# Kernel tuning notes

Hardware: AMD Instinct MI355X
Metric: run time of the kernel (lower is better)

Reference implementation:

```python
import jax, jax.numpy as jnp
import numpy as np

B, S, T = 64, 128, 64
HD, VS, VT = 1024, 32000, 32000


def setup_inputs() -> dict:
    key = jax.random.key(0)
    ks = jax.random.split(key, 20)
    p = lambda k, shape: (jax.random.normal(k, shape, jnp.float32) * 0.02)
    return {
        "src_nums": jax.random.randint(ks[0], (B, S), 0, VS, dtype=jnp.int32),
        "tgt_nums": jax.random.randint(ks[1], (B, T), 0, VT, dtype=jnp.int32),
        "src_emb": p(ks[2], (VS, HD)),
        "tgt_emb": p(ks[3], (VT, HD)),
        "enc_Wx1": p(ks[4], (HD, 4 * HD)),
        "enc_Wh1": p(ks[5], (HD, 4 * HD)),
        "enc_b1": jnp.zeros((4 * HD,), jnp.float32),
        "enc_Wx2": p(ks[6], (HD, 4 * HD)),
        "enc_Wh2": p(ks[7], (HD, 4 * HD)),
        "enc_b2": jnp.zeros((4 * HD,), jnp.float32),
        "dec_Wx": p(ks[8], (HD, 4 * HD)),
        "dec_Wh": p(ks[9], (HD, 4 * HD)),
        "dec_b": jnp.zeros((4 * HD,), jnp.float32),
        "dec_h0": p(ks[10], (1, HD)),
        "dec_m0": p(ks[11], (1, HD)),
        "Wt": p(ks[12], (2 * HD, HD)),
        "bt": jnp.zeros((HD,), jnp.float32),
        "Wo": p(ks[13], (HD, VT)),
        "bo": jnp.zeros((VT,), jnp.float32),
    }


def _lstm_cell(x, h, c, Wx, Wh, b):
    g = x @ Wx + h @ Wh + b            # [B, 4H], gate order i,f,g,o
    i, f, gg, o = jnp.split(g, 4, axis=-1)
    c = jax.nn.sigmoid(f) * c + jax.nn.sigmoid(i) * jnp.tanh(gg)
    h = jax.nn.sigmoid(o) * jnp.tanh(c)
    return h, c


def reference(src_nums, tgt_nums, src_emb, tgt_emb,
              enc_Wx1, enc_Wh1, enc_b1, enc_Wx2, enc_Wh2, enc_b2,
              dec_Wx, dec_Wh, dec_b, dec_h0, dec_m0, Wt, bt, Wo, bo):
    Bb, Ss = src_nums.shape
    Hd = src_emb.shape[1]
    # ---- Encoder: 2-layer LSTM over source ----
    embs = src_emb[src_nums]                       # [B,S,H]
    z0 = jnp.zeros((Bb, Hd), embs.dtype)

    def enc_step(carry, x):
        h1, c1, h2, c2 = carry
        h1, c1 = _lstm_cell(x, h1, c1, enc_Wx1, enc_Wh1, enc_b1)
        h2, c2 = _lstm_cell(h1, h2, c2, enc_Wx2, enc_Wh2, enc_b2)
        return (h1, c1, h2, c2), h2

    _, Hseq = jax.lax.scan(enc_step, (z0, z0, z0, z0), jnp.swapaxes(embs, 0, 1))
    Henc = jnp.swapaxes(Hseq, 0, 1)                # [B,S,H]
    mask = src_nums == 0                           # pad mask
    scale = 1.0 / jnp.sqrt(jnp.array(Hd, jnp.float32))

    # ---- Decoder: per-step attention + LSTMCell + tanh proj + log-softmax ----
    h = jnp.tile(dec_h0, (Bb, 1))
    m = jnp.tile(dec_m0, (Bb, 1))

    def dec_step(carry, tgt):
        h, m, loss = carry
        scores = jnp.einsum('bd,bsd->bs', h, Henc) * scale
        scores = jnp.where(mask, -jnp.inf, scores)
        a = jax.nn.softmax(scores, axis=-1)
        ctx = jnp.einsum('bs,bsd->bd', a, Henc)
        z = jnp.tanh(jnp.concatenate([ctx, h], axis=-1) @ Wt + bt)
        logp = jax.nn.log_softmax(z @ Wo + bo, axis=-1)    # [B,V]
        tok_lp = jnp.take_along_axis(logp, tgt[:, None], axis=-1)[:, 0]
        loss = loss - jnp.sum(jnp.where(tgt != 0, tok_lp, 0.0))
        x = tgt_emb[tgt]
        h, m = _lstm_cell(x, h, m, dec_Wx, dec_Wh, dec_b)
        return (h, m, loss), None

    (_, _, loss), _ = jax.lax.scan(
        dec_step, (h, m, jnp.float32(0.0)), jnp.swapaxes(tgt_nums, 0, 1))
    return loss
```

## Files before the change

kernel.cpp:

```cpp
#include <hip/hip_runtime.h>


#define Bv 64
#define Sv 128
#define Tv 64
#define Hv 1024
#define H4v 4096
#define Vv 32000
#define NBLK 256

using bf16x8 = __attribute__((ext_vector_type(8))) short;
using f32x4  = __attribute__((ext_vector_type(4))) float;

typedef __attribute__((address_space(1))) const void gvoid_t;
typedef __attribute__((address_space(3))) void lvoid_t;

__device__ __forceinline__ void gload16(const void* g, void* l) {
  __builtin_amdgcn_global_load_lds((gvoid_t*)g, (lvoid_t*)l, 16, 0, 0);
}

__device__ __forceinline__ float bf2f(unsigned short u) {
  unsigned int v = ((unsigned int)u) << 16;
  return __uint_as_float(v);
}
__device__ __forceinline__ unsigned short f2bf(float f) {
  unsigned int u = __float_as_uint(f);
  return (unsigned short)((u + 0x7FFFu + ((u >> 16) & 1u)) >> 16);
}
__device__ __forceinline__ float sigm(float x) { return 1.f / (1.f + __expf(-x)); }
__device__ __forceinline__ float tanh_f(float x) {
  float ax = fabsf(x);
  float e = __expf(-2.f * ax);
  float t = (1.f - e) / (1.f + e);
  return copysignf(t, x);
}

__device__ __forceinline__ int4 ldx4(const unsigned short* p) {
  int4 r;
  asm volatile("global_load_dwordx4 %0, %1, off" : "=v"(r) : "v"(p));
  return r;
}
__device__ __forceinline__ int2 ldx2(const unsigned short* p) {
  int2 r;
  asm volatile("global_load_dwordx2 %0, %1, off" : "=v"(r) : "v"(p));
  return r;
}
__device__ __forceinline__ void stx2u_wt(unsigned short* p, int2 v) {
  asm volatile("global_store_dwordx2 %0, %1, off sc0 sc1" :: "v"(p), "v"(v) : "memory");
}
__device__ __forceinline__ void vm_wait_c(int n) {
  switch (n) {
    case 32: asm volatile("s_waitcnt vmcnt(32)" ::: "memory"); break;
    case 28: asm volatile("s_waitcnt vmcnt(28)" ::: "memory"); break;
    case 24: asm volatile("s_waitcnt vmcnt(24)" ::: "memory"); break;
    case 20: asm volatile("s_waitcnt vmcnt(20)" ::: "memory"); break;
    case 16: asm volatile("s_waitcnt vmcnt(16)" ::: "memory"); break;
    case 12: asm volatile("s_waitcnt vmcnt(12)" ::: "memory"); break;
    case 8:  asm volatile("s_waitcnt vmcnt(8)"  ::: "memory"); break;
    case 4:  asm volatile("s_waitcnt vmcnt(4)"  ::: "memory"); break;
    default: asm volatile("s_waitcnt vmcnt(0)"  ::: "memory"); break;
  }
}

__device__ __forceinline__ void wait_all64(int* f, int tid) {
  if (tid < 64) {
    int it = 0;
    while (true) {
      int v = __hip_atomic_load(f + tid, __ATOMIC_RELAXED, __HIP_MEMORY_SCOPE_AGENT);
      if (__all(v != 0)) break;
      __builtin_amdgcn_s_sleep(2);
      if (++it > (1 << 17)) break;
    }
  }
  __syncthreads();
}
__device__ __forceinline__ void wait_all128(int* f, int tid) {
  if (tid < 64) {
    int it = 0;
    while (true) {
      int a = __hip_atomic_load(f + tid, __ATOMIC_RELAXED, __HIP_MEMORY_SCOPE_AGENT);
      int b = __hip_atomic_load(f + tid + 64, __ATOMIC_RELAXED, __HIP_MEMORY_SCOPE_AGENT);
      if (__all((a != 0) && (b != 0))) break;
      __builtin_amdgcn_s_sleep(2);
      if (++it > (1 << 17)) break;
    }
  }
  __syncthreads();
}
__device__ __forceinline__ void post_flag(int* f, int tid) {
  __syncthreads();
  if (tid == 0) __hip_atomic_store(f, 1, __ATOMIC_RELAXED, __HIP_MEMORY_SCOPE_AGENT);
}

__global__ __launch_bounds__(256) void transpose_bf16(const float* __restrict__ in,
                                                      unsigned short* __restrict__ out,
                                                      int R, int C, int ostride) {
  __shared__ float tile[32][33];
  int tx = threadIdx.x, ty = threadIdx.y;
  int c0 = blockIdx.x * 32, r0 = blockIdx.y * 32;
#pragma unroll
  for (int i = 0; i < 32; i += 8)
    tile[ty + i][tx] = in[(size_t)(r0 + ty + i) * C + c0 + tx];
  __syncthreads();
#pragma unroll
  for (int i = 0; i < 32; i += 8)
    out[(size_t)(c0 + ty + i) * ostride + r0 + tx] = f2bf(tile[tx][ty + i]);
}

__global__ __launch_bounds__(256) void gather_emb(const int* __restrict__ toks,
                                                  const float* __restrict__ emb,
                                                  unsigned short* __restrict__ dst) {
  int r = blockIdx.x, tid = threadIdx.x;
  int tok = toks[r];
  int j = tid * 4;
  float4 v = *(const float4*)&emb[(size_t)tok * Hv + j];
  ushort4 o;
  o.x = f2bf(v.x); o.y = f2bf(v.y); o.z = f2bf(v.z); o.w = f2bf(v.w);
  *(ushort4*)&dst[(size_t)r * Hv + j] = o;
}

__global__ __launch_bounds__(256) void init_k(unsigned short* __restrict__ zhx,
                                              unsigned short* __restrict__ hdx0,
                                              const float* __restrict__ h0,
                                              int* __restrict__ flg) {
  int idx = blockIdx.x * 256 + threadIdx.x;
  int j = idx & (Hv - 1);
  int b = idx >> 10;
  zhx[idx] = 0;
  hdx0[(j >> 4) * 1024 + b * 16 + (j & 15)] = f2bf(h0[j]);
  if (idx < 28672) flg[idx] = 0;
}

template <int EPI>
__global__ __launch_bounds__(256) void gemm128(const unsigned short* __restrict__ A,
                                               const unsigned short* __restrict__ Bt,
                                               const float* __restrict__ bias,
                                               unsigned short* __restrict__ Cbf,
                                               int M, int N, int K,
                                               float* __restrict__ partial,
                                               float* __restrict__ tlog,
                                               const int* __restrict__ tgt) {
  __shared__ unsigned short As[128 * 64];
  __shared__ unsigned short Bs[128 * 64];
  int tid = threadIdx.x, lane = tid & 63, w = tid >> 6;
  int wr = w >> 1, wc = w & 1;
  int m0 = (EPI == 3) ? blockIdx.x * 128 : blockIdx.y * 128;
  int n0 = (EPI == 3) ? blockIdx.y * 128 : blockIdx.x * 128;
  f32x4 acc[4][4] = {};
  for (int k0 = 0; k0 < K; k0 += 64) {
    __syncthreads();
#pragma unroll
    for (int q = 0; q < 4; ++q) {
      int idx = q * 256 + tid;
      int row = idx >> 3, phys = idx & 7, lg = phys ^ (row & 7);
      gload16(A + (size_t)(m0 + row) * K + k0 + lg * 8, &As[idx * 8]);
    }
#pragma unroll
    for (int q = 0; q < 4; ++q) {
      int idx = q * 256 + tid;
      int row = idx >> 3, phys = idx & 7, lg = phys ^ (row & 7);
      gload16(Bt + (size_t)(n0 + row) * K + k0 + lg * 8, &Bs[idx * 8]);
    }
    __syncthreads();
#pragma unroll
    for (int kk = 0; kk < 64; kk += 32) {
      int lgb = (kk >> 3) + (lane >> 4);
      bf16x8 af[4], bfr[4];
#pragma unroll
      for (int m = 0; m < 4; ++m) {
        int row = wr * 64 + m * 16 + (lane & 15);
        af[m] = *(const bf16x8*)&As[(row * 8 + (lgb ^ (row & 7))) * 8];
      }
#pragma unroll
      for (int n = 0; n < 4; ++n) {
        int row = wc * 64 + n * 16 + (lane & 15);
        bfr[n] = *(const bf16x8*)&Bs[(row * 8 + (lgb ^ (row & 7))) * 8];
      }
#pragma unroll
      for (int m = 0; m < 4; ++m)
#pragma unroll
        for (int n = 0; n < 4; ++n)
          acc[m][n] = __builtin_amdgcn_mfma_f32_16x16x32_bf16(af[m], bfr[n], acc[m][n], 0, 0, 0);
    }
  }
  if (EPI == 2) {
#pragma unroll
    for (int m = 0; m < 4; ++m)
#pragma unroll
      for (int n = 0; n < 4; ++n) {
        int col = n0 + wc * 64 + n * 16 + (lane & 15);
        float bv = bias[col];
#pragma unroll
        for (int j = 0; j < 4; ++j) {
          int row = m0 + wr * 64 + m * 16 + (lane >> 4) * 4 + j;
          float v = acc[m][n][j] + bv;
          Cbf[(size_t)row * N + col] = f2bf(tanhf(v));
        }
      }
  } else if (EPI == 3) {
    int chunk = (n0 + wc * 64) >> 6;
#pragma unroll
    for (int m = 0; m < 4; ++m)
#pragma unroll
      for (int j = 0; j < 4; ++j) {
        int row = m0 + wr * 64 + m * 16 + (lane >> 4) * 4 + j;
        int tv = tgt[row];
        float se = 0.f;
#pragma unroll
        for (int n = 0; n < 4; ++n) {
          int col = n0 + wc * 64 + n * 16 + (lane & 15);
          float v = acc[m][n][j] + bias[col];
          se += __expf(v);
          if (col == tv) tlog[row] = v;
        }
        se += __shfl_xor(se, 1);
        se += __shfl_xor(se, 2);
        se += __shfl_xor(se, 4);
        se += __shfl_xor(se, 8);
        if ((lane & 15) == 0) partial[(size_t)chunk * M + row] = se;
      }
  } else {
    constexpr int TTc = (EPI == 4) ? 128 : 64;
#pragma unroll
    for (int m = 0; m < 4; ++m)
#pragma unroll
      for (int n = 0; n < 4; ++n) {
        int col = n0 + wc * 64 + n * 16 + (lane & 15);
        float bv = bias[col];
        int hcol = col & 1023, g = col >> 10;
#pragma unroll
        for (int j = 0; j < 4; ++j) {
          int row = m0 + wr * 64 + m * 16 + (lane >> 4) * 4 + j;
          int t = row % TTc, b = row / TTc;
          float v = acc[m][n][j] + bv;
          Cbf[((((size_t)t * 64 + (hcol >> 4)) * 64 + b) * 16 + (hcol & 15)) * 4 + g] = f2bf(v);
        }
      }
  }
}

template <int GRP>
__device__ __forceinline__ void run8(
    int gid, int tid, const unsigned short* __restrict__ Wg,
    const unsigned short* __restrict__ XPC, const float* __restrict__ eb2,
    const float* __restrict__ m0, const unsigned short* __restrict__ ZHX,
    unsigned short* __restrict__ H1X, unsigned short* __restrict__ H2X,
    unsigned short* __restrict__ HDX,
    int* __restrict__ C1, int* __restrict__ C2, int* __restrict__ CD,
    unsigned short* Wl, float* gl) {
  constexpr int COLS = (GRP == 1) ? 8 : 16;
  constexpr int KD   = (GRP == 1) ? 2048 : 1024;
  constexpr int NKS  = KD / 128;
  constexpr int NFR  = (GRP == 1) ? 2 : 4;
  constexpr int NT   = (GRP == 2) ? 63 : 128;
  constexpr int GPR  = KD / 8;
  constexpr int WROWS = 4 * COLS;
  const int lane = tid & 63, w = tid >> 6, l4 = lane >> 4, l15 = lane & 15;
  const int j0 = gid * COLS;

#pragma unroll
  for (int it = 0; it < (WROWS * GPR) / 256; ++it) {
    int L = it * 256 + tid;
    int row = L / GPR;
    int g = (L % GPR) ^ (row & 7);
    int gate = row / COLS, cl = row % COLS;
    gload16(Wg + (size_t)(gate * 1024 + j0 + cl) * KD + g * 8, Wl + (size_t)L * 8);
  }
  const int rr0 = (GRP == 1) ? (tid >> 3) : (tid >> 4);
  const int cc  = (GRP == 1) ? (tid & 7) : (tid & 15);
  const bool cellact = (GRP != 1) || (tid < 128);
  float cst[4];
#pragma unroll
  for (int c = 0; c < 4; ++c) cst[c] = (GRP == 2) ? m0[j0 + cc] : 0.f;
  float br_[4];
  if (GRP == 1) {
#pragma unroll
    for (int g = 0; g < 4; ++g) br_[g] = eb2[g * 1024 + j0 + cc];
  }
  const int kq16 = w * (KD / 32);

  asm volatile("s_waitcnt vmcnt(0)" ::: "memory");
  __syncthreads();

  int2 xq[4];
  if (GRP != 1) {
    const unsigned short* xb = XPC + ((size_t)0 * 64 + gid) * 4096;
#pragma unroll
    for (int c = 0; c < 4; ++c) xq[c] = ldx2(xb + ((c * 16 + rr0) * 16 + cc) * 4);
  }

  for (int t = 0; t < NT; ++t) {
    if (GRP == 0) {
      if (t > 0) wait_all64(C1 + (t - 1) * 64, tid);
    } else if (GRP == 1) {
      wait_all64(C1 + t * 64, tid);
      if (t > 0) wait_all128(C2 + (t - 1) * 128, tid);
    } else {
      if (t > 0) wait_all64(CD + t * 64, tid);
    }
    const unsigned short* slab;
    int jb;
    if (GRP == 0) {
      slab = (t == 0) ? ZHX : H1X + (size_t)(t - 1) * 65536;
      jb = w * 256;
    } else if (GRP == 2) {
      slab = HDX + (size_t)t * 65536;
      jb = w * 256;
    } else {
      if (w < 2) { slab = H1X + (size_t)t * 65536; jb = w * 512; }
      else {
        slab = (t == 0) ? ZHX : H2X + (size_t)(t - 1) * 65536;
        jb = w * 512 - 1024;
      }
    }
    const unsigned short* rp[4];
#pragma unroll
    for (int m = 0; m < 4; ++m)
      rp[m] = slab + (size_t)((jb >> 4) + (l4 >> 1)) * 1024 + (m * 16 + l15) * 16 + (l4 & 1) * 8;
    int4 afr[8][4];
#pragma unroll
    for (int pk = 0; pk < 8; ++pk)
#pragma unroll
      for (int m = 0; m < 4; ++m) afr[pk][m] = ldx4(rp[m] + pk * 2048);
    bf16x8 wb[2][NFR];
#pragma unroll
    for (int n = 0; n < NFR; ++n) {
      int row = n * 16 + l15;
      wb[0][n] = *(const bf16x8*)&Wl[(size_t)row * KD + (size_t)((kq16 + l4) ^ (row & 7)) * 8];
    }
    f32x4 acc[4][NFR] = {};
#pragma unroll
    for (int ks = 0; ks < NKS; ++ks) {
      if (ks + 1 < NKS) {
#pragma unroll
        for (int n = 0; n < NFR; ++n) {
          int row = n * 16 + l15;
          wb[(ks + 1) & 1][n] = *(const bf16x8*)&Wl[(size_t)row * KD +
              (size_t)((kq16 + (ks + 1) * 4 + l4) ^ (row & 7)) * 8];
        }
      }
      vm_wait_c((GRP == 1) ? (ks <= 8 ? 28 : 60 - 4 * ks) : (28 - 4 * ks));
      __builtin_amdgcn_sched_barrier(0);
#pragma unroll
      for (int m = 0; m < 4; ++m)
#pragma unroll
        for (int n = 0; n < NFR; ++n)
          acc[m][n] = __builtin_amdgcn_mfma_f32_16x16x32_bf16(
              *(const bf16x8*)&afr[ks & 7][m], wb[ks & 1][n], acc[m][n], 0, 0, 0);
      if (GRP == 1 && ks < 8) {
#pragma unroll
        for (int m = 0; m < 4; ++m) afr[ks & 7][m] = ldx4(rp[m] + (ks + 8) * 2048);
      }
    }
    unsigned short* outp;
    if (GRP == 0)      outp = H1X + (size_t)t * 65536 + gid * 1024;
    else if (GRP == 2) outp = HDX + (size_t)(t + 1) * 65536 + gid * 1024;
    else               outp = H2X + (size_t)t * 65536 + (size_t)(j0 >> 4) * 1024 + (j0 & 8);
    unsigned short ho[4];
#pragma unroll
    for (int c = 0; c < 4; ++c) {
#pragma unroll
      for (int n = 0; n < NFR; ++n)
#pragma unroll
        for (int j = 0; j < 4; ++j) {
          int ric = l4 * 4 + j;
          int col = n * 16 + l15;
          gl[(w * 16 + ric) * 64 + (col ^ ((ric * 4) & 63))] = acc[c][n][j];
        }
      __syncthreads();
      if (cellact) {
        float G[4];
#pragma unroll
        for (int g = 0; g < 4; ++g) {
          int sw = (g * COLS + cc) ^ ((rr0 * 4) & 63);
          G[g] = gl[(0 * 16 + rr0) * 64 + sw] + gl[(1 * 16 + rr0) * 64 + sw] +
                 gl[(2 * 16 + rr0) * 64 + sw] + gl[(3 * 16 + rr0) * 64 + sw];
        }
        float gi, gf, gg, go;
        if (GRP == 1) {
          gi = G[0] + br_[0]; gf = G[1] + br_[1]; gg = G[2] + br_[2]; go = G[3] + br_[3];
        } else {
          gi = G[0] + bf2f((unsigned short)(xq[c].x & 0xFFFF));
          gf = G[1] + bf2f((unsigned short)((unsigned)xq[c].x >> 16));
          gg = G[2] + bf2f((unsigned short)(xq[c].y & 0xFFFF));
          go = G[3] + bf2f((unsigned short)((unsigned)xq[c].y >> 16));
        }
        float cn = sigm(gf) * cst[c] + sigm(gi) * tanh_f(gg);
        float hn = sigm(go) * tanh_f(cn);
        cst[c] = cn;
        ho[c] = f2bf(hn);
      }
      __syncthreads();
    }
    unsigned short* hb = (unsigned short*)gl;
    if (cellact) {
#pragma unroll
      for (int c = 0; c < 4; ++c) hb[(c * 16 + rr0) * COLS + cc] = ho[c];
    }
    __syncthreads();
    if (GRP != 1) {
      int b2 = tid >> 2, q4 = (tid & 3) * 4;
      ushort4 hv = *(const ushort4*)&hb[b2 * 16 + q4];
      int2 pk;
      pk.x = (int)hv.x | ((int)hv.y << 16);
      pk.y = (int)hv.z | ((int)hv.w << 16);
      stx2u_wt(outp + b2 * 16 + q4, pk);
    } else if (tid < 128) {
      int b2 = tid >> 1, q4 = (tid & 1) * 4;
      ushort4 hv = *(const ushort4*)&hb[b2 * 8 + q4];
      int2 pk;
      pk.x = (int)hv.x | ((int)hv.y << 16);
      pk.y = (int)hv.z | ((int)hv.w << 16);
      stx2u_wt(outp + b2 * 16 + q4, pk);
    }
    if (GRP != 1) {
      int tn = (t + 1 < NT) ? (t + 1) : (NT - 1);
      const unsigned short* xb = XPC + ((size_t)tn * 64 + gid) * 4096;
#pragma unroll
      for (int c = 0; c < 4; ++c) xq[c] = ldx2(xb + ((c * 16 + rr0) * 16 + cc) * 4);
      vm_wait_c(4);
    } else {
      asm volatile("s_waitcnt vmcnt(0)" ::: "memory");
    }
    if (GRP == 0)      post_flag(C1 + t * 64 + gid, tid);
    else if (GRP == 1) post_flag(C2 + t * 128 + gid, tid);
    else               post_flag(CD + (t + 1) * 64 + gid, tid);
  }
}

__global__ __launch_bounds__(256, 1) void chain_kernel(
    const unsigned short* __restrict__ W1T, const unsigned short* __restrict__ W2S,
    const unsigned short* __restrict__ WDT, const unsigned short* __restrict__ XPC1,
    const unsigned short* __restrict__ XPCD, const float* __restrict__ eb2,
    const float* __restrict__ m0, const unsigned short* __restrict__ ZHX,
    unsigned short* __restrict__ H1X, unsigned short* __restrict__ H2X,
    unsigned short* __restrict__ HDX, int* __restrict__ flg) {
  __shared__ unsigned short Wl[65536];
  __shared__ float gl[4 * 16 * 64];
  int bid = blockIdx.x, tid = threadIdx.x;
  int* C1 = flg;
  int* C2 = flg + 8192;
  int* CD = flg + 24576;
  if (bid < 64)
    run8<0>(bid, tid, W1T, XPC1, eb2, nullptr, ZHX, H1X, H2X, HDX, C1, C2, CD, Wl, gl);
  else if (bid < 192)
    run8<1>(bid - 64, tid, W2S, nullptr, eb2, nullptr, ZHX, H1X, H2X, HDX, C1, C2, CD, Wl, gl);
  else
    run8<2>(bid - 192, tid, WDT, XPCD, eb2, m0, ZHX, H1X, H2X, HDX, C1, C2, CD, Wl, gl);
}

__global__ __launch_bounds__(256) void reshape_h(const unsigned short* __restrict__ H2X,
                                                 const unsigned short* __restrict__ HDX,
                                                 unsigned short* __restrict__ HENC,
                                                 unsigned short* __restrict__ HDEC) {
  int row = blockIdx.x, tid = threadIdx.x;
  int g = tid >> 2, c = (tid & 3) * 4;
  if (row < Bv * Sv) {
    int b = row >> 7, s = row & 127;
    ushort4 v = *(const ushort4*)&H2X[(size_t)s * 65536 + g * 1024 + b * 16 + c];
    *(ushort4*)&HENC[(size_t)row * Hv + tid * 4] = v;
  } else {
    int r2 = row - Bv * Sv;
    int b = r2 >> 6, t = r2 & 63;
    ushort4 v = *(const ushort4*)&HDX[(size_t)t * 65536 + g * 1024 + b * 16 + c];
    *(ushort4*)&HDEC[(size_t)r2 * Hv + tid * 4] = v;
  }
}

__global__ __launch_bounds__(256) void attn_kernel(const unsigned short* __restrict__ Hdec,
                                                   const unsigned short* __restrict__ Henc,
                                                   const int* __restrict__ src_nums,
                                                   unsigned short* __restrict__ cat) {
  __shared__ float hd[Hv];
  __shared__ float sc[Sv];
  __shared__ float al[Sv];
  __shared__ float inv_s;
  int r = blockIdx.x;
  int b = r >> 6;
  int tid = threadIdx.x;
#pragma unroll
  for (int i = 0; i < 4; ++i) {
    int j = i * 256 + tid;
    hd[j] = bf2f(Hdec[(size_t)r * Hv + j]);
  }
  __syncthreads();
  int lane = tid & 63, w = tid >> 6;
  {
    int s = w * 32 + (lane >> 1);
    int half = lane & 1;
    const unsigned short* hrow = Henc + ((size_t)(b * Sv + s)) * Hv + half * 512;
    const float* hdp = hd + half * 512;
    float ps = 0.f;
#pragma unroll 8
    for (int j = 0; j < 512; j += 2) {
      unsigned int u = *(const unsigned int*)&hrow[j];
      ps += hdp[j] * bf2f((unsigned short)(u & 0xFFFFu));
      ps += hdp[j + 1] * bf2f((unsigned short)(u >> 16));
    }
    ps += __shfl_xor(ps, 1);
    if (half == 0) {
      float v = ps * 0.03125f;
      if (src_nums[b * Sv + s] == 0) v = -1e30f;
      sc[s] = v;
    }
  }
  __syncthreads();
  if (w == 0) {
    float v0 = sc[lane], v1 = sc[lane + 64];
    float mx = fmaxf(v0, v1);
#pragma unroll
    for (int o = 1; o < 64; o <<= 1) mx = fmaxf(mx, __shfl_xor(mx, o));
    float e0 = __expf(v0 - mx), e1 = __expf(v1 - mx);
    al[lane] = e0;
    al[lane + 64] = e1;
    float ss = e0 + e1;
#pragma unroll
    for (int o = 1; o < 64; o <<= 1) ss += __shfl_xor(ss, o);
    if (lane == 0) inv_s = 1.f / ss;
  }
  __syncthreads();
  float inv = inv_s;
  int j0 = tid * 4;
  float a0 = 0, a1 = 0, a2 = 0, a3 = 0;
  for (int s2 = 0; s2 < Sv; ++s2) {
    float a = al[s2];
    const unsigned short* hr = Henc + ((size_t)(b * Sv + s2)) * Hv + j0;
    ushort4 u = *(const ushort4*)hr;
    a0 += a * bf2f(u.x);
    a1 += a * bf2f(u.y);
    a2 += a * bf2f(u.z);
    a3 += a * bf2f(u.w);
  }
  ushort4 o4;
  o4.x = f2bf(a0 * inv); o4.y = f2bf(a1 * inv); o4.z = f2bf(a2 * inv); o4.w = f2bf(a3 * inv);
  *(ushort4*)&cat[(size_t)r * 2048 + j0] = o4;
  ushort4 h4;
  h4.x = f2bf(hd[j0]); h4.y = f2bf(hd[j0 + 1]); h4.z = f2bf(hd[j0 + 2]); h4.w = f2bf(hd[j0 + 3]);
  *(ushort4*)&cat[(size_t)r * 2048 + 1024 + j0] = h4;
}

__global__ __launch_bounds__(256) void loss_row(const float* __restrict__ partial,
                                                const float* __restrict__ tlog,
                                                const int* __restrict__ tgt,
                                                float* __restrict__ rowloss) {
  int r = blockIdx.x * 256 + threadIdx.x;
  float ssum = 0.f;
  for (int c = 0; c < Vv / 64; ++c) ssum += partial[(size_t)c * (Bv * Tv) + r];
  float l = logf(ssum) - tlog[r];
  rowloss[r] = (tgt[r] != 0) ? l : 0.f;
}

__global__ __launch_bounds__(256) void loss_final(const float* __restrict__ rowloss,
                                                  float* __restrict__ out) {
  __shared__ float red[256];
  int tid = threadIdx.x;
  float s = 0.f;
  for (int i = tid; i < Bv * Tv; i += 256) s += rowloss[i];
  red[tid] = s;
  __syncthreads();
  for (int o = 128; o > 0; o >>= 1) {
    if (tid < o) red[tid] += red[tid + o];
    __syncthreads();
  }
  if (tid == 0) out[0] = red[0];
}

extern "C" void kernel_launch(void* const* d_in, const int* in_sizes, int n_in,
                              void* d_out, int out_size, void* d_ws, size_t ws_size,
                              hipStream_t stream) {
  (void)in_sizes; (void)n_in; (void)out_size; (void)ws_size;
  const int* src_nums = (const int*)d_in[0];
  const int* tgt_nums = (const int*)d_in[1];
  const float* src_emb = (const float*)d_in[2];
  const float* tgt_emb = (const float*)d_in[3];
  const float* eWx1 = (const float*)d_in[4];
  const float* eWh1 = (const float*)d_in[5];
  const float* eb1  = (const float*)d_in[6];
  const float* eWx2 = (const float*)d_in[7];
  const float* eWh2 = (const float*)d_in[8];
  const float* eb2  = (const float*)d_in[9];
  const float* dWx  = (const float*)d_in[10];
  const float* dWh  = (const float*)d_in[11];
  const float* db   = (const float*)d_in[12];
  const float* h0   = (const float*)d_in[13];
  const float* m0   = (const float*)d_in[14];
  const float* Wt   = (const float*)d_in[15];
  const float* bt   = (const float*)d_in[16];
  const float* Wo   = (const float*)d_in[17];
  const float* bo   = (const float*)d_in[18];

  char* base = (char*)d_ws;
  size_t off = 0;
  auto alloc = [&](size_t bytes) -> void* {
    void* r = base + off;
    off += (bytes + 255) & ~(size_t)255;
    return r;
  };
  unsigned short* WX1T = (unsigned short*)alloc((size_t)H4v * Hv * 2);
  unsigned short* W1T  = (unsigned short*)alloc((size_t)H4v * Hv * 2);
  unsigned short* W2S  = (unsigned short*)alloc((size_t)H4v * 2048 * 2);
  unsigned short* DWXT = (unsigned short*)alloc((size_t)H4v * Hv * 2);
  unsigned short* WDT  = (unsigned short*)alloc((size_t)H4v * Hv * 2);
  unsigned short* WTT  = (unsigned short*)alloc((size_t)Hv * 2048 * 2);
  unsigned short* WOT  = (unsigned short*)alloc((size_t)Vv * Hv * 2);
  unsigned short* SEMB = (unsigned short*)alloc((size_t)Bv * Sv * Hv * 2);
  unsigned short* TEMB = (unsigned short*)alloc((size_t)Bv * Tv * Hv * 2);
  unsigned short* XPC1 = (unsigned short*)alloc((size_t)Bv * Sv * H4v * 2);
  unsigned short* XPCD = (unsigned short*)alloc((size_t)Bv * Tv * H4v * 2);
  unsigned short* HENC = (unsigned short*)alloc((size_t)Bv * Sv * Hv * 2);
  unsigned short* HDEC = (unsigned short*)alloc((size_t)Bv * Tv * Hv * 2);
  unsigned short* H1X  = (unsigned short*)alloc((size_t)Sv * Bv * Hv * 2);
  unsigned short* H2X  = (unsigned short*)alloc((size_t)Sv * Bv * Hv * 2);
  unsigned short* HDX  = (unsigned short*)alloc((size_t)Tv * Bv * Hv * 2);
  unsigned short* ZHX  = (unsigned short*)alloc((size_t)Bv * Hv * 2);
  unsigned short* CAT  = (unsigned short*)alloc((size_t)Bv * Tv * 2048 * 2);
  unsigned short* ZBUF = (unsigned short*)alloc((size_t)Bv * Tv * Hv * 2);
  float* PART  = (float*)alloc((size_t)(Vv / 64) * (Bv * Tv) * 4);
  float* TLOG  = (float*)alloc((size_t)(Bv * Tv) * 4);
  float* RLOSS = (float*)alloc((size_t)(Bv * Tv) * 4);
  int* FLG     = (int*)alloc(28672 * 4);

  dim3 tb(32, 8);
  transpose_bf16<<<dim3(H4v / 32, Hv / 32), tb, 0, stream>>>(eWx1, WX1T, Hv, H4v, Hv);
  transpose_bf16<<<dim3(H4v / 32, Hv / 32), tb, 0, stream>>>(eWh1, W1T, Hv, H4v, Hv);
  transpose_bf16<<<dim3(H4v / 32, Hv / 32), tb, 0, stream>>>(eWx2, W2S, Hv, H4v, 2048);
  transpose_bf16<<<dim3(H4v / 32, Hv / 32), tb, 0, stream>>>(eWh2, W2S + 1024, Hv, H4v, 2048);
  transpose_bf16<<<dim3(H4v / 32, Hv / 32), tb, 0, stream>>>(dWx, DWXT, Hv, H4v, Hv);
  transpose_bf16<<<dim3(H4v / 32, Hv / 32), tb, 0, stream>>>(dWh, WDT, Hv, H4v, Hv);
  transpose_bf16<<<dim3(Hv / 32, 2048 / 32), tb, 0, stream>>>(Wt, WTT, 2048, Hv, 2048);
  transpose_bf16<<<dim3(Vv / 32, Hv / 32), tb, 0, stream>>>(Wo, WOT, Hv, Vv, Hv);

  init_k<<<256, 256, 0, stream>>>(ZHX, HDX, h0, FLG);
  gather_emb<<<Bv * Sv, 256, 0, stream>>>(src_nums, src_emb, SEMB);
  gather_emb<<<Bv * Tv, 256, 0, stream>>>(tgt_nums, tgt_emb, TEMB);

  gemm128<4><<<dim3(H4v / 128, (Bv * Sv) / 128), 256, 0, stream>>>(
      SEMB, WX1T, eb1, XPC1, Bv * Sv, H4v, Hv, nullptr, nullptr, nullptr);
  gemm128<5><<<dim3(H4v / 128, (Bv * Tv) / 128), 256, 0, stream>>>(
      TEMB, DWXT, db, XPCD, Bv * Tv, H4v, Hv, nullptr, nullptr, nullptr);

  chain_kernel<<<NBLK, 256, 0, stream>>>(W1T, W2S, WDT, XPC1, XPCD, eb2, m0, ZHX, H1X, H2X,
                                         HDX, FLG);

  reshape_h<<<Bv * Sv + Bv * Tv, 256, 0, stream>>>(H2X, HDX, HENC, HDEC);

  attn_kernel<<<Bv * Tv, 256, 0, stream>>>(HDEC, HENC, src_nums, CAT);
  gemm128<2><<<dim3(Hv / 128, (Bv * Tv) / 128), 256, 0, stream>>>(
      CAT, WTT, bt, ZBUF, Bv * Tv, Hv, 2048, nullptr, nullptr, nullptr);
  gemm128<3><<<dim3((Bv * Tv) / 128, Vv / 128), 256, 0, stream>>>(
      ZBUF, WOT, bo, nullptr, Bv * Tv, Vv, Hv, PART, TLOG, tgt_nums);
  loss_row<<<(Bv * Tv) / 256, 256, 0, stream>>>(PART, TLOG, tgt_nums, RLOSS);
  loss_final<<<1, 256, 0, stream>>>(RLOSS, (float*)d_out);
}
```

Before: 1.820 ms.

## Add double-buffered 256x256 GEMM and drop reshape by reading interleaved hidden layout

Replaces the 128x128 GEMM with a 512-thread 256x256-tile kernel that double-buffers LDS and prefetches the next K tile in quarters during MFMA work. It uses a swizzled block order and applies to the input projections and the large vocab projection. It also removes the reshape_h kernel: attention now reads the chain kernel's interleaved H2X/HDX layout directly. The aim is more data reuse per tile and less latency exposure in the dominant output GEMM, plus one fewer kernel and copy. The costs are higher register and LDS pressure and strided attention reads.

```diff
diff --git a/kernel.cpp b/kernel.cpp
--- a/kernel.cpp
+++ b/kernel.cpp
@@ -50,7 +50,6 @@
 }
 __device__ __forceinline__ void vm_wait_c(int n) {
   switch (n) {
-    case 32: asm volatile("s_waitcnt vmcnt(32)" ::: "memory"); break;
     case 28: asm volatile("s_waitcnt vmcnt(28)" ::: "memory"); break;
     case 24: asm volatile("s_waitcnt vmcnt(24)" ::: "memory"); break;
     case 20: asm volatile("s_waitcnt vmcnt(20)" ::: "memory"); break;
@@ -131,21 +130,16 @@
   if (idx < 28672) flg[idx] = 0;
 }
 
-template <int EPI>
-__global__ __launch_bounds__(256) void gemm128(const unsigned short* __restrict__ A,
-                                               const unsigned short* __restrict__ Bt,
-                                               const float* __restrict__ bias,
-                                               unsigned short* __restrict__ Cbf,
-                                               int M, int N, int K,
-                                               float* __restrict__ partial,
-                                               float* __restrict__ tlog,
-                                               const int* __restrict__ tgt) {
+__global__ __launch_bounds__(256) void gemm128_tanh(const unsigned short* __restrict__ A,
+                                                    const unsigned short* __restrict__ Bt,
+                                                    const float* __restrict__ bias,
+                                                    unsigned short* __restrict__ Cbf,
+                                                    int M, int N, int K) {
   __shared__ unsigned short As[128 * 64];
   __shared__ unsigned short Bs[128 * 64];
   int tid = threadIdx.x, lane = tid & 63, w = tid >> 6;
   int wr = w >> 1, wc = w & 1;
-  int m0 = (EPI == 3) ? blockIdx.x * 128 : blockIdx.y * 128;
-  int n0 = (EPI == 3) ? blockIdx.y * 128 : blockIdx.x * 128;
+  int m0 = blockIdx.y * 128, n0 = blockIdx.x * 128;
   f32x4 acc[4][4] = {};
   for (int k0 = 0; k0 < K; k0 += 64) {
     __syncthreads();
@@ -183,33 +177,113 @@
           acc[m][n] = __builtin_amdgcn_mfma_f32_16x16x32_bf16(af[m], bfr[n], acc[m][n], 0, 0, 0);
     }
   }
-  if (EPI == 2) {
-#pragma unroll
-    for (int m = 0; m < 4; ++m)
-#pragma unroll
-      for (int n = 0; n < 4; ++n) {
-        int col = n0 + wc * 64 + n * 16 + (lane & 15);
-        float bv = bias[col];
-#pragma unroll
-        for (int j = 0; j < 4; ++j) {
-          int row = m0 + wr * 64 + m * 16 + (lane >> 4) * 4 + j;
-          float v = acc[m][n][j] + bv;
-          Cbf[(size_t)row * N + col] = f2bf(tanhf(v));
-        }
-      }
-  } else if (EPI == 3) {
-    int chunk = (n0 + wc * 64) >> 6;
-#pragma unroll
-    for (int m = 0; m < 4; ++m)
+#pragma unroll
+  for (int m = 0; m < 4; ++m)
+#pragma unroll
+    for (int n = 0; n < 4; ++n) {
+      int col = n0 + wc * 64 + n * 16 + (lane & 15);
+      float bv = bias[col];
 #pragma unroll
       for (int j = 0; j < 4; ++j) {
         int row = m0 + wr * 64 + m * 16 + (lane >> 4) * 4 + j;
+        Cbf[(size_t)row * N + col] = f2bf(tanhf(acc[m][n][j] + bv));
+      }
+    }
+}
+
+template <int EPI>
+__global__ __launch_bounds__(512, 2) void gemm256(const unsigned short* __restrict__ A,
+                                                  const unsigned short* __restrict__ Bt,
+                                                  const float* __restrict__ bias,
+                                                  unsigned short* __restrict__ Cbf,
+                                                  int M, int N, int K, int MT,
+                                                  float* __restrict__ partial,
+                                                  float* __restrict__ tlog,
+                                                  const int* __restrict__ tgt) {
+  __shared__ unsigned short LB[2][32768];
+  const int tid = threadIdx.x, lane = tid & 63, w = tid >> 6;
+  const int wm = w >> 2, wn = w & 3;
+  const int l15 = lane & 15, hi = lane >> 4;
+  int nwg = gridDim.x;
+  int swz = (blockIdx.x & 7) * (nwg >> 3) + (blockIdx.x >> 3);
+  const int m0 = (swz % MT) * 256;
+  const int n0 = (swz / MT) * 256;
+  const int NKT = K >> 6;
+
+  auto stage_half = [&](int kt, int h) {
+    int bsel = kt & 1;
+    int k0 = kt * 64;
+#pragma unroll
+    for (int rep = 0; rep < 2; ++rep) {
+      int pg = (h & 1) * 1024 + rep * 512 + tid;
+      int row = pg >> 3, pk = pg & 7, kg = pk ^ (row & 7);
+      if (h < 2)
+        gload16(A + (size_t)(m0 + row) * K + k0 + kg * 8, &LB[bsel][pg * 8]);
+      else
+        gload16(Bt + (size_t)(n0 + row) * K + k0 + kg * 8, &LB[bsel][16384 + pg * 8]);
+    }
+  };
+
+#pragma unroll
+  for (int h = 0; h < 4; ++h) stage_half(0, h);
+  asm volatile("s_waitcnt vmcnt(0)" ::: "memory");
+  __syncthreads();
+
+  f32x4 acc[8][4] = {};
+  const int ar7 = l15 & 7;
+  for (int kt = 0; kt < NKT; ++kt) {
+    const unsigned short* buf = LB[kt & 1];
+#pragma unroll
+    for (int q = 0; q < 4; ++q) {
+      const int mq = q & 1, nq = q >> 1;
+      bf16x8 af[4][2], bf[2][2];
+#pragma unroll
+      for (int mf = 0; mf < 4; ++mf) {
+        int row = wm * 128 + (mq * 4 + mf) * 16 + l15;
+#pragma unroll
+        for (int ks = 0; ks < 2; ++ks)
+          af[mf][ks] = *(const bf16x8*)&buf[(row * 8 + ((ks * 4 + hi) ^ ar7)) * 8];
+      }
+#pragma unroll
+      for (int nf = 0; nf < 2; ++nf) {
+        int row = wn * 64 + (nq * 2 + nf) * 16 + l15;
+#pragma unroll
+        for (int ks = 0; ks < 2; ++ks)
+          bf[nf][ks] = *(const bf16x8*)&buf[16384 + (row * 8 + ((ks * 4 + hi) ^ ar7)) * 8];
+      }
+      if (kt + 1 < NKT) stage_half(kt + 1, q);
+      asm volatile("s_waitcnt lgkmcnt(8)" ::: "memory");
+      __builtin_amdgcn_s_barrier();
+      asm volatile("s_waitcnt lgkmcnt(0)" ::: "memory");
+      __builtin_amdgcn_sched_barrier(0);
+      __builtin_amdgcn_s_setprio(1);
+#pragma unroll
+      for (int ks = 0; ks < 2; ++ks)
+#pragma unroll
+        for (int mf = 0; mf < 4; ++mf)
+#pragma unroll
+          for (int nf = 0; nf < 2; ++nf)
+            acc[mq * 4 + mf][nq * 2 + nf] = __builtin_amdgcn_mfma_f32_16x16x32_bf16(
+                af[mf][ks], bf[nf][ks], acc[mq * 4 + mf][nq * 2 + nf], 0, 0, 0);
+      __builtin_amdgcn_s_setprio(0);
+      if (q == 3) asm volatile("s_waitcnt vmcnt(0)" ::: "memory");
+      __builtin_amdgcn_s_barrier();
+    }
+  }
+
+  if (EPI == 3) {
+    int chunk = (n0 + wn * 64) >> 6;
+#pragma unroll
+    for (int mf = 0; mf < 8; ++mf)
+#pragma unroll
+      for (int j = 0; j < 4; ++j) {
+        int row = m0 + wm * 128 + mf * 16 + hi * 4 + j;
         int tv = tgt[row];
         float se = 0.f;
 #pragma unroll
-        for (int n = 0; n < 4; ++n) {
-          int col = n0 + wc * 64 + n * 16 + (lane & 15);
-          float v = acc[m][n][j] + bias[col];
+        for (int nf = 0; nf < 4; ++nf) {
+          int col = n0 + wn * 64 + nf * 16 + l15;
+          float v = acc[mf][nf][j] + bias[col];
           se += __expf(v);
           if (col == tv) tlog[row] = v;
         }
@@ -217,22 +291,22 @@
         se += __shfl_xor(se, 2);
         se += __shfl_xor(se, 4);
         se += __shfl_xor(se, 8);
-        if ((lane & 15) == 0) partial[(size_t)chunk * M + row] = se;
+        if (l15 == 0) partial[(size_t)chunk * M + row] = se;
       }
   } else {
     constexpr int TTc = (EPI == 4) ? 128 : 64;
 #pragma unroll
-    for (int m = 0; m < 4; ++m)
-#pragma unroll
-      for (int n = 0; n < 4; ++n) {
-        int col = n0 + wc * 64 + n * 16 + (lane & 15);
+    for (int mf = 0; mf < 8; ++mf)
+#pragma unroll
+      for (int nf = 0; nf < 4; ++nf) {
+        int col = n0 + wn * 64 + nf * 16 + l15;
         float bv = bias[col];
         int hcol = col & 1023, g = col >> 10;
 #pragma unroll
         for (int j = 0; j < 4; ++j) {
-          int row = m0 + wr * 64 + m * 16 + (lane >> 4) * 4 + j;
+          int row = m0 + wm * 128 + mf * 16 + hi * 4 + j;
           int t = row % TTc, b = row / TTc;
-          float v = acc[m][n][j] + bv;
+          float v = acc[mf][nf][j] + bv;
           Cbf[((((size_t)t * 64 + (hcol >> 4)) * 64 + b) * 16 + (hcol & 15)) * 4 + g] = f2bf(v);
         }
       }
@@ -449,26 +523,8 @@
     run8<2>(bid - 192, tid, WDT, XPCD, eb2, m0, ZHX, H1X, H2X, HDX, C1, C2, CD, Wl, gl);
 }
 
-__global__ __launch_bounds__(256) void reshape_h(const unsigned short* __restrict__ H2X,
-                                                 const unsigned short* __restrict__ HDX,
-                                                 unsigned short* __restrict__ HENC,
-                                                 unsigned short* __restrict__ HDEC) {
-  int row = blockIdx.x, tid = threadIdx.x;
-  int g = tid >> 2, c = (tid & 3) * 4;
-  if (row < Bv * Sv) {
-    int b = row >> 7, s = row & 127;
-    ushort4 v = *(const ushort4*)&H2X[(size_t)s * 65536 + g * 1024 + b * 16 + c];
-    *(ushort4*)&HENC[(size_t)row * Hv + tid * 4] = v;
-  } else {
-    int r2 = row - Bv * Sv;
-    int b = r2 >> 6, t = r2 & 63;
-    ushort4 v = *(const ushort4*)&HDX[(size_t)t * 65536 + g * 1024 + b * 16 + c];
-    *(ushort4*)&HDEC[(size_t)r2 * Hv + tid * 4] = v;
-  }
-}
-
-__global__ __launch_bounds__(256) void attn_kernel(const unsigned short* __restrict__ Hdec,
-                                                   const unsigned short* __restrict__ Henc,
+__global__ __launch_bounds__(256) void attn_kernel(const unsigned short* __restrict__ HDX,
+                                                   const unsigned short* __restrict__ H2X,
                                                    const int* __restrict__ src_nums,
                                                    unsigned short* __restrict__ cat) {
   __shared__ float hd[Hv];
@@ -476,24 +532,25 @@
   __shared__ float al[Sv];
   __shared__ float inv_s;
   int r = blockIdx.x;
-  int b = r >> 6;
+  int b = r >> 6, t = r & 63;
   int tid = threadIdx.x;
 #pragma unroll
   for (int i = 0; i < 4; ++i) {
     int j = i * 256 + tid;
-    hd[j] = bf2f(Hdec[(size_t)r * Hv + j]);
+    hd[j] = bf2f(HDX[(size_t)t * 65536 + (j >> 4) * 1024 + b * 16 + (j & 15)]);
   }
   __syncthreads();
   int lane = tid & 63, w = tid >> 6;
   {
     int s = w * 32 + (lane >> 1);
     int half = lane & 1;
-    const unsigned short* hrow = Henc + ((size_t)(b * Sv + s)) * Hv + half * 512;
+    const unsigned short* sb = H2X + (size_t)s * 65536 + b * 16;
     const float* hdp = hd + half * 512;
     float ps = 0.f;
 #pragma unroll 8
     for (int j = 0; j < 512; j += 2) {
-      unsigned int u = *(const unsigned int*)&hrow[j];
+      int e = half * 512 + j;
+      unsigned int u = *(const unsigned int*)&sb[(e >> 4) * 1024 + (e & 15)];
       ps += hdp[j] * bf2f((unsigned short)(u & 0xFFFFu));
       ps += hdp[j + 1] * bf2f((unsigned short)(u >> 16));
     }
@@ -521,11 +578,11 @@
   __syncthreads();
   float inv = inv_s;
   int j0 = tid * 4;
+  int soff = (j0 >> 4) * 1024 + b * 16 + (j0 & 15);
   float a0 = 0, a1 = 0, a2 = 0, a3 = 0;
   for (int s2 = 0; s2 < Sv; ++s2) {
     float a = al[s2];
-    const unsigned short* hr = Henc + ((size_t)(b * Sv + s2)) * Hv + j0;
-    ushort4 u = *(const ushort4*)hr;
+    ushort4 u = *(const ushort4*)&H2X[(size_t)s2 * 65536 + soff];
     a0 += a * bf2f(u.x);
     a1 += a * bf2f(u.y);
     a2 += a * bf2f(u.z);
@@ -607,8 +664,6 @@
   unsigned short* TEMB = (unsigned short*)alloc((size_t)Bv * Tv * Hv * 2);
   unsigned short* XPC1 = (unsigned short*)alloc((size_t)Bv * Sv * H4v * 2);
   unsigned short* XPCD = (unsigned short*)alloc((size_t)Bv * Tv * H4v * 2);
-  unsigned short* HENC = (unsigned short*)alloc((size_t)Bv * Sv * Hv * 2);
-  unsigned short* HDEC = (unsigned short*)alloc((size_t)Bv * Tv * Hv * 2);
   unsigned short* H1X  = (unsigned short*)alloc((size_t)Sv * Bv * Hv * 2);
   unsigned short* H2X  = (unsigned short*)alloc((size_t)Sv * Bv * Hv * 2);
   unsigned short* HDX  = (unsigned short*)alloc((size_t)Tv * Bv * Hv * 2);
@@ -634,21 +689,19 @@
   gather_emb<<<Bv * Sv, 256, 0, stream>>>(src_nums, src_emb, SEMB);
   gather_emb<<<Bv * Tv, 256, 0, stream>>>(tgt_nums, tgt_emb, TEMB);
 
-  gemm128<4><<<dim3(H4v / 128, (Bv * Sv) / 128), 256, 0, stream>>>(
-      SEMB, WX1T, eb1, XPC1, Bv * Sv, H4v, Hv, nullptr, nullptr, nullptr);
-  gemm128<5><<<dim3(H4v / 128, (Bv * Tv) / 128), 256, 0, stream>>>(
-      TEMB, DWXT, db, XPCD, Bv * Tv, H4v, Hv, nullptr, nullptr, nullptr);
+  gemm256<4><<<(Bv * Sv / 256) * (H4v / 256), 512, 0, stream>>>(
+      SEMB, WX1T, eb1, XPC1, Bv * Sv, H4v, Hv, Bv * Sv / 256, nullptr, nullptr, nullptr);
+  gemm256<5><<<(Bv * Tv / 256) * (H4v / 256), 512, 0, stream>>>(
+      TEMB, DWXT, db, XPCD, Bv * Tv, H4v, Hv, Bv * Tv / 256, nullptr, nullptr, nullptr);
 
   chain_kernel<<<NBLK, 256, 0, stream>>>(W1T, W2S, WDT, XPC1, XPCD, eb2, m0, ZHX, H1X, H2X,
                                          HDX, FLG);
 
-  reshape_h<<<Bv * Sv + Bv * Tv, 256, 0, stream>>>(H2X, HDX, HENC, HDEC);
-
-  attn_kernel<<<Bv * Tv, 256, 0, stream>>>(HDEC, HENC, src_nums, CAT);
-  gemm128<2><<<dim3(Hv / 128, (Bv * Tv) / 128), 256, 0, stream>>>(
-      CAT, WTT, bt, ZBUF, Bv * Tv, Hv, 2048, nullptr, nullptr, nullptr);
-  gemm128<3><<<dim3((Bv * Tv) / 128, Vv / 128), 256, 0, stream>>>(
-      ZBUF, WOT, bo, nullptr, Bv * Tv, Vv, Hv, PART, TLOG, tgt_nums);
+  attn_kernel<<<Bv * Tv, 256, 0, stream>>>(HDX, H2X, src_nums, CAT);
+  gemm128_tanh<<<dim3(Hv / 128, (Bv * Tv) / 128), 256, 0, stream>>>(
+      CAT, WTT, bt, ZBUF, Bv * Tv, Hv, 2048);
+  gemm256<3><<<(Bv * Tv / 256) * (Vv / 256), 512, 0, stream>>>(
+      ZBUF, WOT, bo, nullptr, Bv * Tv, Vv, Hv, Bv * Tv / 256, PART, TLOG, tgt_nums);
   loss_row<<<(Bv * Tv) / 256, 256, 0, stream>>>(PART, TLOG, tgt_nums, RLOSS);
   loss_final<<<1, 256, 0, stream>>>(RLOSS, (float*)d_out);
 }
```

Result: slower. 1.981 ms (+8.8%).
